# Kernel optimization log

Measured on AMD Instinct MI355X. Metric: run time of the kernel, lower is better.

## Reference

```python
import jax, jax.numpy as jnp
import numpy as np

X_CH, Y_CH, DIM, NUM_HEAD = 256, 512, 128, 4
H_DIM = DIM // NUM_HEAD
GAMMA = H_DIM ** (-0.5)


def conv1x1(x, w, b):
    # x: [B,C,H,W], w: [O,C], b: [O]
    return jnp.einsum('bchw,oc->bohw', x, w) + b[None, :, None, None]


def _split_qkv(qkv, bs, hw):
    # qkv: [B, 3*DIM, H, W] -> q,k,v each [B, NUM_HEAD, HW, H_DIM]
    qkv = qkv.reshape(bs, 3, NUM_HEAD, H_DIM, hw)
    qkv = jnp.transpose(qkv, (1, 0, 2, 4, 3))  # [3, B, H, HW, D]
    return qkv[0], qkv[1], qkv[2]


def setup_inputs() -> dict:
    key = jax.random.key(0)
    ks = jax.random.split(key, 12)
    s = lambda fan_in: 1.0 / np.sqrt(fan_in)
    x = jax.random.normal(ks[0], (2, X_CH, 64, 64), dtype=jnp.float32)
    y = jax.random.normal(ks[1], (2, Y_CH, 32, 32), dtype=jnp.float32)
    wx_qkv = jax.random.normal(ks[2], (3 * DIM, X_CH), dtype=jnp.float32) * s(X_CH)
    bx_qkv = jax.random.normal(ks[3], (3 * DIM,), dtype=jnp.float32) * s(X_CH)
    wy_qkv = jax.random.normal(ks[4], (3 * DIM, Y_CH), dtype=jnp.float32) * s(Y_CH)
    by_qkv = jax.random.normal(ks[5], (3 * DIM,), dtype=jnp.float32) * s(Y_CH)
    wpx = jax.random.normal(ks[6], (X_CH, DIM), dtype=jnp.float32) * s(DIM)
    bpx = jax.random.normal(ks[7], (X_CH,), dtype=jnp.float32) * s(DIM)
    wpy = jax.random.normal(ks[8], (Y_CH, DIM), dtype=jnp.float32) * s(DIM)
    bpy = jax.random.normal(ks[9], (Y_CH,), dtype=jnp.float32) * s(DIM)
    return {"x": x, "y": y, "wx_qkv": wx_qkv, "bx_qkv": bx_qkv,
            "wy_qkv": wy_qkv, "by_qkv": by_qkv,
            "wpx": wpx, "bpx": bpx, "wpy": wpy, "bpy": bpy}


def reference(x, y, wx_qkv, bx_qkv, wy_qkv, by_qkv, wpx, bpx, wpy, bpy):
    bs, _, h_x, w_x = x.shape
    _, _, h_y, w_y = y.shape
    hw_x, hw_y = h_x * w_x, h_y * w_y

    q_x, k_x, v_x = _split_qkv(conv1x1(x, wx_qkv, bx_qkv), bs, hw_x)
    q_y, k_y, v_y = _split_qkv(conv1x1(y, wy_qkv, by_qkv), bs, hw_y)

    # x attends to y
    atten_x = jax.nn.softmax(jnp.einsum('bhqd,bhkd->bhqk', q_x, k_y) * GAMMA, axis=-1)
    out_x = jnp.einsum('bhqk,bhkd->bhqd', atten_x, v_y)  # [B,H,HWx,D]
    out_x = jnp.transpose(out_x, (0, 1, 3, 2)).reshape(bs, DIM, h_x, w_x)

    # y attends to x
    atten_y = jax.nn.softmax(jnp.einsum('bhqd,bhkd->bhqk', q_y, k_x) * GAMMA, axis=-1)
    out_y = jnp.einsum('bhqk,bhkd->bhqd', atten_y, v_x)
    out_y = jnp.transpose(out_y, (0, 1, 3, 2)).reshape(bs, DIM, h_y, w_y)

    out_x = conv1x1(out_x, wpx, bpx) + x
    out_y = conv1x1(out_y, wpy, bpy) + y
    return out_x, out_y
```

## Files before the change

kernel.cpp:

```cpp
#include <hip/hip_runtime.h>
#include <hip/hip_bf16.h>
#include <cstdint>

#define B 2
#define NH 4
#define HD 32
#define DIM 128
#define CX 256
#define CY 512
#define PX 4096
#define PY 1024
#define QKV 384
#define GAMMA 0.17677669529663687f

typedef unsigned short u16;
typedef unsigned int u32;

using short8 = __attribute__((ext_vector_type(8))) short;
using f32x4  = __attribute__((ext_vector_type(4))) float;

__device__ __forceinline__ float bf2f(u32 h) {
  union { u32 u; float f; } v; v.u = (h & 0xffffu) << 16; return v.f;
}
__device__ __forceinline__ u16 f2bf(float f) {
  u32 u = __float_as_uint(f);
  u32 r = (u + 0x7fffu + ((u >> 16) & 1u)) >> 16;
  return (u16)r;
}
__device__ __forceinline__ bool is_f32(const void* src) {
  u32 u = ((const u16*)src)[2 * (threadIdx.x & 63)];
  return __ballot((u & 0x7F80u) >= 0x4600u) != 0ull;
}

#define N_X   (B * CX * PX)
#define N_Y   (B * CY * PY)
#define N_WX  (QKV * CX)
#define N_BX  (QKV)
#define N_WY  (QKV * CY)
#define N_BY  (QKV)
#define N_WPX (CX * DIM)
#define N_BPX (CX)
#define N_WPY (CY * DIM)
#define N_BPY (CY)

enum : size_t {
  OFF_CWX   = 0,
  OFF_CBX   = OFF_CWX  + N_WX,
  OFF_CWY   = OFF_CBX  + N_BX,
  OFF_CBY   = OFF_CWY  + N_WY,
  OFF_CWPX  = OFF_CBY  + N_BY,
  OFF_CBPX  = OFF_CWPX + N_WPX,
  OFF_CWPY  = OFF_CBPX + N_BPX,
  OFF_CBPY  = OFF_CWPY + N_WPY,
  OFF_XT    = OFF_CBPY + N_BPY,
  OFF_YT    = OFF_XT   + (size_t)B * PX * CX,
  OFF_QPX   = OFF_YT   + (size_t)B * PY * CY,
  OFF_KPX   = OFF_QPX  + (size_t)B * NH * PX * HD,
  OFF_QPY   = OFF_KPX  + (size_t)B * NH * PX * HD,
  OFF_KPY   = OFF_QPY  + (size_t)B * NH * PY * HD,
  OFF_VCX   = OFF_KPY  + (size_t)B * NH * PY * HD,
  OFF_VCY   = OFF_VCX  + (size_t)B * DIM * PX,
  OFF_OTX   = OFF_VCY  + (size_t)B * DIM * PY,
  OFF_OTY   = OFF_OTX  + (size_t)B * PX * DIM,
  WS_END    = OFF_OTY  + (size_t)B * PY * DIM,
};

#define XPX_BLKS 512
#define XPY_BLKS 256
__global__ __launch_bounds__(256) void k_prep(
    const void* x, const void* y, const void* wx, const void* bx,
    const void* wy, const void* by, const void* wpx, const void* bpx,
    const void* wpy, const void* bpy, u16* __restrict__ ws) {
  const int id = blockIdx.x;
  if (id < XPX_BLKS + XPY_BLKS) {
    __shared__ u16 tile[64][68];
    const void* src; u16* dst; int C, P, p_t, c_t, b;
    if (id < XPX_BLKS) {
      src = x; dst = ws + OFF_XT; C = CX; P = PX;
      p_t = id & 63; c_t = (id >> 6) & 3; b = id >> 8;
    } else {
      int id2 = id - XPX_BLKS;
      src = y; dst = ws + OFF_YT; C = CY; P = PY;
      p_t = id2 & 15; c_t = (id2 >> 4) & 7; b = id2 >> 7;
    }
    const bool f32in = is_f32(src);
    const int tx = threadIdx.x & 15, tc = threadIdx.x >> 4;
    const int p0 = p_t * 64, c0 = c_t * 64;
#pragma unroll
    for (int i = 0; i < 4; i++) {
      int cl = tc + i * 16;
      size_t sidx = ((size_t)b * C + c0 + cl) * P + p0 + tx * 4;
      u16 v0, v1, v2, v3;
      if (f32in) {
        float4 f = *(const float4*)((const float*)src + sidx);
        v0 = f2bf(f.x); v1 = f2bf(f.y); v2 = f2bf(f.z); v3 = f2bf(f.w);
      } else {
        uint2 u = *(const uint2*)((const u16*)src + sidx);
        v0 = (u16)u.x; v1 = (u16)(u.x >> 16); v2 = (u16)u.y; v3 = (u16)(u.y >> 16);
      }
      tile[tx * 4 + 0][cl] = v0; tile[tx * 4 + 1][cl] = v1;
      tile[tx * 4 + 2][cl] = v2; tile[tx * 4 + 3][cl] = v3;
    }
    __syncthreads();
#pragma unroll
    for (int i = 0; i < 4; i++) {
      int pl = tc + i * 16;
      *(uint2*)&dst[((size_t)b * P + p0 + pl) * C + c0 + tx * 4] =
          *(const uint2*)&tile[pl][tx * 4];
    }
  } else {
    int wid = id - (XPX_BLKS + XPY_BLKS);
    const void* src; size_t dstoff; int n, base;
    if      (wid < 48)  { src = wx;  dstoff = OFF_CWX;  n = N_WX;  base = 0; }
    else if (wid < 49)  { src = bx;  dstoff = OFF_CBX;  n = N_BX;  base = 48; }
    else if (wid < 145) { src = wy;  dstoff = OFF_CWY;  n = N_WY;  base = 49; }
    else if (wid < 146) { src = by;  dstoff = OFF_CBY;  n = N_BY;  base = 145; }
    else if (wid < 162) { src = wpx; dstoff = OFF_CWPX; n = N_WPX; base = 146; }
    else if (wid < 163) { src = bpx; dstoff = OFF_CBPX; n = N_BPX; base = 162; }
    else if (wid < 195) { src = wpy; dstoff = OFF_CWPY; n = N_WPY; base = 163; }
    else                { src = bpy; dstoff = OFF_CBPY; n = N_BPY; base = 195; }
    const bool f32in = is_f32(src);
    int e0 = (wid - base) * 2048 + threadIdx.x * 8;
    if (e0 >= n) return;
    u16* dst = ws + dstoff + e0;
    if (f32in) {
      const float* s = (const float*)src + e0;
      float4 a = *(const float4*)s;
      float4 bq = *(const float4*)(s + 4);
      ushort4 o0, o1;
      o0.x = f2bf(a.x);  o0.y = f2bf(a.y);  o0.z = f2bf(a.z);  o0.w = f2bf(a.w);
      o1.x = f2bf(bq.x); o1.y = f2bf(bq.y); o1.z = f2bf(bq.z); o1.w = f2bf(bq.w);
      *(ushort4*)dst = o0;
      *(ushort4*)(dst + 4) = o1;
    } else {
      uint4 v = *(const uint4*)((const u16*)src + e0);
      *(uint4*)dst = v;
    }
  }
}

__global__ __launch_bounds__(256) void k_qkv(u16* __restrict__ ws) {
  const int t = threadIdx.x;
  const int lane = t & 63, w = t >> 6;
  const int ql = lane & 15, quad = lane >> 4;
  const int b = blockIdx.z;

  const u16 *W, *Xt, *bias; u16 *qp, *kp, *vc; int C, P, pxb;
  if (blockIdx.x < 64) {
    W = ws + OFF_CWX; Xt = ws + OFF_XT; bias = ws + OFF_CBX;
    qp = ws + OFF_QPX; kp = ws + OFF_KPX; vc = ws + OFF_VCX;
    C = CX; P = PX; pxb = blockIdx.x;
  } else {
    W = ws + OFF_CWY; Xt = ws + OFF_YT; bias = ws + OFF_CBY;
    qp = ws + OFF_QPY; kp = ws + OFF_KPY; vc = ws + OFF_VCY;
    C = CY; P = PY; pxb = blockIdx.x - 64;
  }
  const int p_w = pxb * 64 + (w & 1) * 32;
  const int o_w = blockIdx.y * 64 + (w >> 1) * 32;

  const u16* wr0 = W + (size_t)(o_w + ql) * C;
  const u16* wr1 = W + (size_t)(o_w + 16 + ql) * C;
  const u16* xr0 = Xt + ((size_t)b * P + p_w + ql) * C;
  const u16* xr1 = Xt + ((size_t)b * P + p_w + 16 + ql) * C;

  union U { uint4 u; short8 s; };
  f32x4 acc[2][2];
#pragma unroll
  for (int i = 0; i < 2; i++)
#pragma unroll
    for (int j = 0; j < 2; j++) acc[i][j] = (f32x4){0.f, 0.f, 0.f, 0.f};

  U a0, a1, b0, b1, a0n, a1n, b0n, b1n;
  {
    int off = quad * 8;
    a0.u = *(const uint4*)&wr0[off];
    a1.u = *(const uint4*)&wr1[off];
    b0.u = *(const uint4*)&xr0[off];
    b1.u = *(const uint4*)&xr1[off];
  }

  const bool isv = blockIdx.y >= 4;
  if (!isv) {
#pragma unroll 4
    for (int c0 = 0; c0 < C; c0 += 32) {
      if (c0 + 32 < C) {
        int off = c0 + 32 + quad * 8;
        a0n.u = *(const uint4*)&wr0[off];
        a1n.u = *(const uint4*)&wr1[off];
        b0n.u = *(const uint4*)&xr0[off];
        b1n.u = *(const uint4*)&xr1[off];
      }
      acc[0][0] = __builtin_amdgcn_mfma_f32_16x16x32_bf16(a0.s, b0.s, acc[0][0], 0, 0, 0);
      acc[0][1] = __builtin_amdgcn_mfma_f32_16x16x32_bf16(a0.s, b1.s, acc[0][1], 0, 0, 0);
      acc[1][0] = __builtin_amdgcn_mfma_f32_16x16x32_bf16(a1.s, b0.s, acc[1][0], 0, 0, 0);
      acc[1][1] = __builtin_amdgcn_mfma_f32_16x16x32_bf16(a1.s, b1.s, acc[1][1], 0, 0, 0);
      a0 = a0n; a1 = a1n; b0 = b0n; b1 = b1n;
    }
  } else {
#pragma unroll 4
    for (int c0 = 0; c0 < C; c0 += 32) {
      if (c0 + 32 < C) {
        int off = c0 + 32 + quad * 8;
        a0n.u = *(const uint4*)&wr0[off];
        a1n.u = *(const uint4*)&wr1[off];
        b0n.u = *(const uint4*)&xr0[off];
        b1n.u = *(const uint4*)&xr1[off];
      }
      acc[0][0] = __builtin_amdgcn_mfma_f32_16x16x32_bf16(b0.s, a0.s, acc[0][0], 0, 0, 0);
      acc[0][1] = __builtin_amdgcn_mfma_f32_16x16x32_bf16(b1.s, a0.s, acc[0][1], 0, 0, 0);
      acc[1][0] = __builtin_amdgcn_mfma_f32_16x16x32_bf16(b0.s, a1.s, acc[1][0], 0, 0, 0);
      acc[1][1] = __builtin_amdgcn_mfma_f32_16x16x32_bf16(b1.s, a1.s, acc[1][1], 0, 0, 0);
      a0 = a0n; a1 = a1n; b0 = b0n; b1 = b1n;
    }
  }

  if (!isv) {
    float bs[2][4];
#pragma unroll
    for (int oi = 0; oi < 2; oi++)
#pragma unroll
      for (int r = 0; r < 4; r++)
        bs[oi][r] = bf2f(bias[o_w + oi * 16 + quad * 4 + r]);
    bool isq = blockIdx.y < 2;
    float scale = isq ? GAMMA : 1.0f;
    u16* dstT = isq ? qp : kp;
#pragma unroll
    for (int oi = 0; oi < 2; oi++)
#pragma unroll
      for (int pi = 0; pi < 2; pi++) {
        int p = p_w + pi * 16 + ql;
        int o = o_w + oi * 16 + quad * 4 - (isq ? 0 : 128);
        int hh = o >> 5, d = o & 31;
        f32x4 a = acc[oi][pi];
        uint2 pk;
        pk.x = (u32)f2bf((a[0] + bs[oi][0]) * scale) |
               ((u32)f2bf((a[1] + bs[oi][1]) * scale) << 16);
        pk.y = (u32)f2bf((a[2] + bs[oi][2]) * scale) |
               ((u32)f2bf((a[3] + bs[oi][3]) * scale) << 16);
        *(uint2*)&dstT[((size_t)(b * NH + hh) * P + p) * HD + d] = pk;
      }
  } else {
#pragma unroll
    for (int oi = 0; oi < 2; oi++) {
      int o = o_w + oi * 16 + ql - 256;
      float bv = bf2f(bias[o_w + oi * 16 + ql]);
#pragma unroll
      for (int pi = 0; pi < 2; pi++) {
        int pbase = p_w + pi * 16 + quad * 4;
        f32x4 a = acc[oi][pi];
        ushort4 st;
        st.x = f2bf(a[0] + bv); st.y = f2bf(a[1] + bv);
        st.z = f2bf(a[2] + bv); st.w = f2bf(a[3] + bv);
        *(ushort4*)&vc[((size_t)b * DIM + o) * P + pbase] = st;
      }
    }
  }
}

template <int NQF, int KW>
__device__ __forceinline__ void attn_core(
    const u16* __restrict__ Qp, const u16* __restrict__ Kp,
    const u16* __restrict__ Vc, u16* __restrict__ Ot, int Pq, int Pk,
    int q0, int h, int b, u16* pool, float (*lfb)[64]) {
  const int t = threadIdx.x;
  const int lane = t & 63, w = t >> 6;
  const int ql = lane & 15, quad = lane >> 4;

  union U { uint4 u; short8 s; };
  U qf[NQF];
#pragma unroll
  for (int qi = 0; qi < NQF; qi++)
    qf[qi].u = *(const uint4*)&Qp[((size_t)(b * NH + h) * Pq + q0 + qi * 16 + ql) * HD + quad * 8];

  const int kspan = Pk >> 2;
  const int kk0 = w * kspan;
  const int niter = kspan / KW;
  const int f0 = ((ql >> 2) << 3) | (ql & 3);

  const u16* kbase = Kp + ((size_t)(b * NH + h) * Pk + kk0 + f0) * HD + quad * 8;
  const u16* v0base = Vc + ((size_t)(b * DIM + h * HD + ql)) * Pk + kk0 + quad * 8;
  const u16* v1base = v0base + (size_t)16 * Pk;

  f32x4 o0[NQF], o1[NQF];
  float l_run[NQF];
#pragma unroll
  for (int qi = 0; qi < NQF; qi++) {
    o0[qi] = (f32x4){0.f, 0.f, 0.f, 0.f};
    o1[qi] = (f32x4){0.f, 0.f, 0.f, 0.f};
    l_run[qi] = 0.f;
  }

  auto step32 = [&](U& xka, U& xkb, U& xva, U& xvb) {
#pragma unroll
    for (int qi = 0; qi < NQF; qi++) {
      f32x4 z = {0.f, 0.f, 0.f, 0.f};
      f32x4 st0 = __builtin_amdgcn_mfma_f32_16x16x32_bf16(xka.s, qf[qi].s, z, 0, 0, 0);
      f32x4 st1 = __builtin_amdgcn_mfma_f32_16x16x32_bf16(xkb.s, qf[qi].s, z, 0, 0, 0);

      float p[8];
#pragma unroll
      for (int r = 0; r < 4; r++) { p[r] = __expf(st0[r]); p[4 + r] = __expf(st1[r]); }
      l_run[qi] += ((p[0] + p[1]) + (p[2] + p[3])) + ((p[4] + p[5]) + (p[6] + p[7]));

      U pf;
      pf.u.x = __builtin_amdgcn_perm(__float_as_uint(p[1]), __float_as_uint(p[0]), 0x07060302u);
      pf.u.y = __builtin_amdgcn_perm(__float_as_uint(p[3]), __float_as_uint(p[2]), 0x07060302u);
      pf.u.z = __builtin_amdgcn_perm(__float_as_uint(p[5]), __float_as_uint(p[4]), 0x07060302u);
      pf.u.w = __builtin_amdgcn_perm(__float_as_uint(p[7]), __float_as_uint(p[6]), 0x07060302u);

      o0[qi] = __builtin_amdgcn_mfma_f32_16x16x32_bf16(xva.s, pf.s, o0[qi], 0, 0, 0);
      o1[qi] = __builtin_amdgcn_mfma_f32_16x16x32_bf16(xvb.s, pf.s, o1[qi], 0, 0, 0);
    }
  };

  U ka, kb, va, vb, kan, kbn, van, vbn;
  U kc, kd, vc, vd, kcn, kdn, vcn, vdn;
  ka.u = *(const uint4*)&kbase[0];
  kb.u = *(const uint4*)&kbase[4 * HD];
  va.u = *(const uint4*)&v0base[0];
  vb.u = *(const uint4*)&v1base[0];
  if constexpr (KW == 64) {
    kc.u = *(const uint4*)&kbase[32 * HD];
    kd.u = *(const uint4*)&kbase[36 * HD];
    vc.u = *(const uint4*)&v0base[32];
    vd.u = *(const uint4*)&v1base[32];
  }

  for (int it = 0; it < niter; it++) {
    if (it + 1 < niter) {
      size_t go = (size_t)(it + 1) * KW;
      kan.u = *(const uint4*)&kbase[go * HD];
      kbn.u = *(const uint4*)&kbase[(go + 4) * HD];
      van.u = *(const uint4*)&v0base[go];
      vbn.u = *(const uint4*)&v1base[go];
      if constexpr (KW == 64) {
        kcn.u = *(const uint4*)&kbase[(go + 32) * HD];
        kdn.u = *(const uint4*)&kbase[(go + 36) * HD];
        vcn.u = *(const uint4*)&v0base[go + 32];
        vdn.u = *(const uint4*)&v1base[go + 32];
      }
    }

    step32(ka, kb, va, vb);
    if constexpr (KW == 64) step32(kc, kd, vc, vd);

    ka = kan; kb = kbn; va = van; vb = vbn;
    if constexpr (KW == 64) { kc = kcn; kd = kdn; vc = vcn; vd = vdn; }
  }

#pragma unroll
  for (int qi = 0; qi < NQF; qi++) {
    float l = l_run[qi];
    l += __shfl_xor(l, 16);
    l += __shfl_xor(l, 32);
    l_run[qi] = l;
  }

  float* Of = (float*)(pool + (size_t)w * 4096);
#pragma unroll
  for (int qi = 0; qi < NQF; qi++) {
#pragma unroll
    for (int r = 0; r < 4; r++) {
      Of[(qi * 16 + ql) * 32 + quad * 4 + r] = o0[qi][r];
      Of[(qi * 16 + ql) * 32 + 16 + quad * 4 + r] = o1[qi][r];
    }
    if (quad == 0) lfb[w][qi * 16 + ql] = l_run[qi];
  }
  __syncthreads();

  const float* OfA = (const float*)pool;
#pragma unroll
  for (int k = 0; k < NQF * 2; k++) {
    int e = t + k * 256;
    int q = e >> 5, d = e & 31;
    float lt = lfb[0][q] + lfb[1][q] + lfb[2][q] + lfb[3][q];
    int di = q * 32 + d;
    float v = (OfA[di] + OfA[2048 + di]) + (OfA[4096 + di] + OfA[6144 + di]);
    Ot[((size_t)b * Pq + q0 + q) * DIM + h * HD + d] = f2bf(v / lt);
  }
}

__global__ __launch_bounds__(256) void k_attn(u16* __restrict__ ws) {
  __shared__ __align__(16) u16 pool[16384];
  __shared__ float lfb[4][64];
  const int c = blockIdx.x & 7;
  const int j = blockIdx.x >> 3;
  const int b = c >> 2, h = c & 3;
  if (j < 32) {
    attn_core<2, 64>(ws + OFF_QPY, ws + OFF_KPX, ws + OFF_VCX, ws + OFF_OTY,
                     PY, PX, j * 32, h, b, pool, lfb);
  } else {
    attn_core<4, 32>(ws + OFF_QPX, ws + OFF_KPY, ws + OFF_VCY, ws + OFF_OTX,
                     PX, PY, (j - 32) * 64, h, b, pool, lfb);
  }
}

__global__ __launch_bounds__(256) void k_proj(
    u16* __restrict__ ws, void* __restrict__ outv,
    const void* __restrict__ resx, const void* __restrict__ resy) {
  const int u = blockIdx.x;
  const u16 *W, *A, *bias; const void* res; int OT, P, pxb, byi, b; size_t out_off;
  if (u < 512) {
    W = ws + OFF_CWPX; A = ws + OFF_OTX; bias = ws + OFF_CBPX;
    res = resx; OT = CX; P = PX; out_off = 0;
    pxb = u & 63; byi = (u >> 6) & 3; b = u >> 8;
  } else {
    int v = u - 512;
    W = ws + OFF_CWPY; A = ws + OFF_OTY; bias = ws + OFF_CBPY;
    res = resy; OT = CY; P = PY; out_off = (size_t)B * CX * PX;
    pxb = v & 15; byi = (v >> 4) & 7; b = v >> 7;
  }
  const bool f32io = is_f32(res);
  const int t = threadIdx.x;
  const int lane = t & 63, w = t >> 6;
  const int ql = lane & 15, quad = lane >> 4;
  const int p_w = pxb * 64 + (w & 1) * 32;
  const int o_w = byi * 64 + (w >> 1) * 32;

  const u16* wr0 = W + (size_t)(o_w + ql) * DIM;
  const u16* wr1 = W + (size_t)(o_w + 16 + ql) * DIM;
  const u16* xr0 = A + ((size_t)b * P + p_w + ql) * DIM;
  const u16* xr1 = A + ((size_t)b * P + p_w + 16 + ql) * DIM;

  union U { uint4 u; short8 s; };
  U wa0[4], wa1[4], xb0[4], xb1[4];
#pragma unroll
  for (int i = 0; i < 4; i++) {
    int off = i * 32 + quad * 8;
    wa0[i].u = *(const uint4*)&wr0[off];
    wa1[i].u = *(const uint4*)&wr1[off];
    xb0[i].u = *(const uint4*)&xr0[off];
    xb1[i].u = *(const uint4*)&xr1[off];
  }

  f32x4 acc[2][2];
#pragma unroll
  for (int i = 0; i < 2; i++)
#pragma unroll
    for (int j = 0; j < 2; j++) acc[i][j] = (f32x4){0.f, 0.f, 0.f, 0.f};

#pragma unroll
  for (int i = 0; i < 4; i++) {
    acc[0][0] = __builtin_amdgcn_mfma_f32_16x16x32_bf16(xb0[i].s, wa0[i].s, acc[0][0], 0, 0, 0);
    acc[0][1] = __builtin_amdgcn_mfma_f32_16x16x32_bf16(xb1[i].s, wa0[i].s, acc[0][1], 0, 0, 0);
    acc[1][0] = __builtin_amdgcn_mfma_f32_16x16x32_bf16(xb0[i].s, wa1[i].s, acc[1][0], 0, 0, 0);
    acc[1][1] = __builtin_amdgcn_mfma_f32_16x16x32_bf16(xb1[i].s, wa1[i].s, acc[1][1], 0, 0, 0);
  }

#pragma unroll
  for (int oi = 0; oi < 2; oi++) {
    int o = o_w + oi * 16 + ql;
    float bv = bf2f(bias[o]);
#pragma unroll
    for (int pi = 0; pi < 2; pi++) {
      int pbase = p_w + pi * 16 + quad * 4;
      size_t idx = ((size_t)b * OT + o) * P + pbase;
      f32x4 a = acc[oi][pi];
      if (f32io) {
        float4 rv = *(const float4*)((const float*)res + idx);
        float4 ov;
        ov.x = a[0] + bv + rv.x; ov.y = a[1] + bv + rv.y;
        ov.z = a[2] + bv + rv.z; ov.w = a[3] + bv + rv.w;
        *(float4*)((float*)outv + out_off + idx) = ov;
      } else {
        ushort4 rv = *(const ushort4*)((const u16*)res + idx);
        ushort4 ov;
        ov.x = f2bf(a[0] + bv + bf2f(rv.x));
        ov.y = f2bf(a[1] + bv + bf2f(rv.y));
        ov.z = f2bf(a[2] + bv + bf2f(rv.z));
        ov.w = f2bf(a[3] + bv + bf2f(rv.w));
        *(ushort4*)((u16*)outv + out_off + idx) = ov;
      }
    }
  }
}

extern "C" void kernel_launch(void* const* d_in, const int* in_sizes, int n_in,
                              void* d_out, int out_size, void* d_ws, size_t ws_size,
                              hipStream_t stream) {
  (void)in_sizes; (void)n_in; (void)out_size; (void)ws_size;
  u16* ws = (u16*)d_ws;

  k_prep<<<dim3(XPX_BLKS + XPY_BLKS + 196), 256, 0, stream>>>(
      d_in[0], d_in[1], d_in[2], d_in[3], d_in[4], d_in[5],
      d_in[6], d_in[7], d_in[8], d_in[9], ws);
  k_qkv<<<dim3(80, 6, B), 256, 0, stream>>>(ws);
  k_attn<<<dim3(768), 256, 0, stream>>>(ws);
  k_proj<<<dim3(768), 256, 0, stream>>>(ws, d_out, d_in[0], d_in[1]);
}
```

Baseline: 135.2 us.

## Fuse input transpose and bf16 conversion into QKV and projection kernels

Removes the separate prep kernel that converted x, y and the weights to bf16 and transposed the activations into workspace. The QKV kernel now loads raw input tiles, converts and transposes them through double-buffered shared memory, and converts fp32 weights to bf16 on the fly. The projection kernel also reads fp32 weights and biases directly. This saves one launch and a full round trip of the activations through global memory. In exchange the weights are converted redundantly in every block and a barrier is added per 64-channel chunk.

```diff
diff --git a/kernel.cpp b/kernel.cpp
--- a/kernel.cpp
+++ b/kernel.cpp
@@ -32,29 +32,8 @@
   return __ballot((u & 0x7F80u) >= 0x4600u) != 0ull;
 }
 
-#define N_X   (B * CX * PX)
-#define N_Y   (B * CY * PY)
-#define N_WX  (QKV * CX)
-#define N_BX  (QKV)
-#define N_WY  (QKV * CY)
-#define N_BY  (QKV)
-#define N_WPX (CX * DIM)
-#define N_BPX (CX)
-#define N_WPY (CY * DIM)
-#define N_BPY (CY)
-
 enum : size_t {
-  OFF_CWX   = 0,
-  OFF_CBX   = OFF_CWX  + N_WX,
-  OFF_CWY   = OFF_CBX  + N_BX,
-  OFF_CBY   = OFF_CWY  + N_WY,
-  OFF_CWPX  = OFF_CBY  + N_BY,
-  OFF_CBPX  = OFF_CWPX + N_WPX,
-  OFF_CWPY  = OFF_CBPX + N_BPX,
-  OFF_CBPY  = OFF_CWPY + N_WPY,
-  OFF_XT    = OFF_CBPY + N_BPY,
-  OFF_YT    = OFF_XT   + (size_t)B * PX * CX,
-  OFF_QPX   = OFF_YT   + (size_t)B * PY * CY,
+  OFF_QPX   = 0,
   OFF_KPX   = OFF_QPX  + (size_t)B * NH * PX * HD,
   OFF_QPY   = OFF_KPX  + (size_t)B * NH * PX * HD,
   OFF_KPY   = OFF_QPY  + (size_t)B * NH * PY * HD,
@@ -65,153 +44,129 @@
   WS_END    = OFF_OTY  + (size_t)B * PY * DIM,
 };
 
-#define XPX_BLKS 512
-#define XPY_BLKS 256
-__global__ __launch_bounds__(256) void k_prep(
-    const void* x, const void* y, const void* wx, const void* bx,
-    const void* wy, const void* by, const void* wpx, const void* bpx,
-    const void* wpy, const void* bpy, u16* __restrict__ ws) {
-  const int id = blockIdx.x;
-  if (id < XPX_BLKS + XPY_BLKS) {
-    __shared__ u16 tile[64][68];
-    const void* src; u16* dst; int C, P, p_t, c_t, b;
-    if (id < XPX_BLKS) {
-      src = x; dst = ws + OFF_XT; C = CX; P = PX;
-      p_t = id & 63; c_t = (id >> 6) & 3; b = id >> 8;
-    } else {
-      int id2 = id - XPX_BLKS;
-      src = y; dst = ws + OFF_YT; C = CY; P = PY;
-      p_t = id2 & 15; c_t = (id2 >> 4) & 7; b = id2 >> 7;
-    }
-    const bool f32in = is_f32(src);
-    const int tx = threadIdx.x & 15, tc = threadIdx.x >> 4;
-    const int p0 = p_t * 64, c0 = c_t * 64;
-#pragma unroll
-    for (int i = 0; i < 4; i++) {
-      int cl = tc + i * 16;
-      size_t sidx = ((size_t)b * C + c0 + cl) * P + p0 + tx * 4;
-      u16 v0, v1, v2, v3;
-      if (f32in) {
-        float4 f = *(const float4*)((const float*)src + sidx);
-        v0 = f2bf(f.x); v1 = f2bf(f.y); v2 = f2bf(f.z); v3 = f2bf(f.w);
-      } else {
-        uint2 u = *(const uint2*)((const u16*)src + sidx);
-        v0 = (u16)u.x; v1 = (u16)(u.x >> 16); v2 = (u16)u.y; v3 = (u16)(u.y >> 16);
-      }
-      tile[tx * 4 + 0][cl] = v0; tile[tx * 4 + 1][cl] = v1;
-      tile[tx * 4 + 2][cl] = v2; tile[tx * 4 + 3][cl] = v3;
-    }
-    __syncthreads();
-#pragma unroll
-    for (int i = 0; i < 4; i++) {
-      int pl = tc + i * 16;
-      *(uint2*)&dst[((size_t)b * P + p0 + pl) * C + c0 + tx * 4] =
-          *(const uint2*)&tile[pl][tx * 4];
-    }
-  } else {
-    int wid = id - (XPX_BLKS + XPY_BLKS);
-    const void* src; size_t dstoff; int n, base;
-    if      (wid < 48)  { src = wx;  dstoff = OFF_CWX;  n = N_WX;  base = 0; }
-    else if (wid < 49)  { src = bx;  dstoff = OFF_CBX;  n = N_BX;  base = 48; }
-    else if (wid < 145) { src = wy;  dstoff = OFF_CWY;  n = N_WY;  base = 49; }
-    else if (wid < 146) { src = by;  dstoff = OFF_CBY;  n = N_BY;  base = 145; }
-    else if (wid < 162) { src = wpx; dstoff = OFF_CWPX; n = N_WPX; base = 146; }
-    else if (wid < 163) { src = bpx; dstoff = OFF_CBPX; n = N_BPX; base = 162; }
-    else if (wid < 195) { src = wpy; dstoff = OFF_CWPY; n = N_WPY; base = 163; }
-    else                { src = bpy; dstoff = OFF_CBPY; n = N_BPY; base = 195; }
-    const bool f32in = is_f32(src);
-    int e0 = (wid - base) * 2048 + threadIdx.x * 8;
-    if (e0 >= n) return;
-    u16* dst = ws + dstoff + e0;
-    if (f32in) {
-      const float* s = (const float*)src + e0;
-      float4 a = *(const float4*)s;
-      float4 bq = *(const float4*)(s + 4);
-      ushort4 o0, o1;
-      o0.x = f2bf(a.x);  o0.y = f2bf(a.y);  o0.z = f2bf(a.z);  o0.w = f2bf(a.w);
-      o1.x = f2bf(bq.x); o1.y = f2bf(bq.y); o1.z = f2bf(bq.z); o1.w = f2bf(bq.w);
-      *(ushort4*)dst = o0;
-      *(ushort4*)(dst + 4) = o1;
-    } else {
-      uint4 v = *(const uint4*)((const u16*)src + e0);
-      *(uint4*)dst = v;
-    }
-  }
-}
-
-__global__ __launch_bounds__(256) void k_qkv(u16* __restrict__ ws) {
+__global__ __launch_bounds__(256) void k_qkv(
+    const void* __restrict__ xin, const void* __restrict__ yin,
+    const void* __restrict__ wxp, const void* __restrict__ bxp,
+    const void* __restrict__ wyp, const void* __restrict__ byp,
+    u16* __restrict__ ws) {
+  __shared__ __align__(16) u16 xt[2][64][68];
   const int t = threadIdx.x;
   const int lane = t & 63, w = t >> 6;
   const int ql = lane & 15, quad = lane >> 4;
   const int b = blockIdx.z;
 
-  const u16 *W, *Xt, *bias; u16 *qp, *kp, *vc; int C, P, pxb;
+  const void *W, *Xsrc, *bias; u16 *qp, *kp, *vc; int C, P, pxb;
   if (blockIdx.x < 64) {
-    W = ws + OFF_CWX; Xt = ws + OFF_XT; bias = ws + OFF_CBX;
+    W = wxp; Xsrc = xin; bias = bxp;
     qp = ws + OFF_QPX; kp = ws + OFF_KPX; vc = ws + OFF_VCX;
     C = CX; P = PX; pxb = blockIdx.x;
   } else {
-    W = ws + OFF_CWY; Xt = ws + OFF_YT; bias = ws + OFF_CBY;
+    W = wyp; Xsrc = yin; bias = byp;
     qp = ws + OFF_QPY; kp = ws + OFF_KPY; vc = ws + OFF_VCY;
     C = CY; P = PY; pxb = blockIdx.x - 64;
   }
-  const int p_w = pxb * 64 + (w & 1) * 32;
+  const bool xf32 = is_f32(Xsrc);
+  const bool wf32 = is_f32(W);
+  const bool bf32 = is_f32(bias);
+  const int NC = C >> 6;
+  const int p0 = pxb * 64;
+  const int pw_loc = (w & 1) * 32;
   const int o_w = blockIdx.y * 64 + (w >> 1) * 32;
-
-  const u16* wr0 = W + (size_t)(o_w + ql) * C;
-  const u16* wr1 = W + (size_t)(o_w + 16 + ql) * C;
-  const u16* xr0 = Xt + ((size_t)b * P + p_w + ql) * C;
-  const u16* xr1 = Xt + ((size_t)b * P + p_w + 16 + ql) * C;
+  const int tx = t & 15, tc = t >> 4;
 
   union U { uint4 u; short8 s; };
+
+  float4 sf[4]; uint2 su[4];
+  auto stage_load = [&](int ci) {
+#pragma unroll
+    for (int i = 0; i < 4; i++) {
+      int cl = tc + i * 16;
+      size_t sidx = ((size_t)b * C + ci * 64 + cl) * P + p0 + tx * 4;
+      if (xf32) sf[i] = *(const float4*)((const float*)Xsrc + sidx);
+      else      su[i] = *(const uint2*)((const u16*)Xsrc + sidx);
+    }
+  };
+  auto stage_write = [&](int buf) {
+#pragma unroll
+    for (int i = 0; i < 4; i++) {
+      int cl = tc + i * 16;
+      if (xf32) {
+        xt[buf][tx * 4 + 0][cl] = f2bf(sf[i].x);
+        xt[buf][tx * 4 + 1][cl] = f2bf(sf[i].y);
+        xt[buf][tx * 4 + 2][cl] = f2bf(sf[i].z);
+        xt[buf][tx * 4 + 3][cl] = f2bf(sf[i].w);
+      } else {
+        xt[buf][tx * 4 + 0][cl] = (u16)su[i].x;
+        xt[buf][tx * 4 + 1][cl] = (u16)(su[i].x >> 16);
+        xt[buf][tx * 4 + 2][cl] = (u16)su[i].y;
+        xt[buf][tx * 4 + 3][cl] = (u16)(su[i].y >> 16);
+      }
+    }
+  };
+
+  auto loadW = [&](int row, int cglob) {
+    U r;
+    if (wf32) {
+      const float* wp = (const float*)W + (size_t)row * C + cglob;
+      float4 lo = *(const float4*)wp;
+      float4 hi = *(const float4*)(wp + 4);
+      r.u.x = (u32)f2bf(lo.x) | ((u32)f2bf(lo.y) << 16);
+      r.u.y = (u32)f2bf(lo.z) | ((u32)f2bf(lo.w) << 16);
+      r.u.z = (u32)f2bf(hi.x) | ((u32)f2bf(hi.y) << 16);
+      r.u.w = (u32)f2bf(hi.z) | ((u32)f2bf(hi.w) << 16);
+    } else {
+      r.u = *(const uint4*)((const u16*)W + (size_t)row * C + cglob);
+    }
+    return r;
+  };
+  auto bval = [&](int o) -> float {
+    return bf32 ? ((const float*)bias)[o] : bf2f(((const u16*)bias)[o]);
+  };
+
   f32x4 acc[2][2];
 #pragma unroll
   for (int i = 0; i < 2; i++)
 #pragma unroll
     for (int j = 0; j < 2; j++) acc[i][j] = (f32x4){0.f, 0.f, 0.f, 0.f};
 
-  U a0, a1, b0, b1, a0n, a1n, b0n, b1n;
-  {
-    int off = quad * 8;
-    a0.u = *(const uint4*)&wr0[off];
-    a1.u = *(const uint4*)&wr1[off];
-    b0.u = *(const uint4*)&xr0[off];
-    b1.u = *(const uint4*)&xr1[off];
-  }
+  stage_load(0);
+  stage_write(0);
+  __syncthreads();
 
   const bool isv = blockIdx.y >= 4;
-  if (!isv) {
-#pragma unroll 4
-    for (int c0 = 0; c0 < C; c0 += 32) {
-      if (c0 + 32 < C) {
-        int off = c0 + 32 + quad * 8;
-        a0n.u = *(const uint4*)&wr0[off];
-        a1n.u = *(const uint4*)&wr1[off];
-        b0n.u = *(const uint4*)&xr0[off];
-        b1n.u = *(const uint4*)&xr1[off];
-      }
-      acc[0][0] = __builtin_amdgcn_mfma_f32_16x16x32_bf16(a0.s, b0.s, acc[0][0], 0, 0, 0);
-      acc[0][1] = __builtin_amdgcn_mfma_f32_16x16x32_bf16(a0.s, b1.s, acc[0][1], 0, 0, 0);
-      acc[1][0] = __builtin_amdgcn_mfma_f32_16x16x32_bf16(a1.s, b0.s, acc[1][0], 0, 0, 0);
-      acc[1][1] = __builtin_amdgcn_mfma_f32_16x16x32_bf16(a1.s, b1.s, acc[1][1], 0, 0, 0);
-      a0 = a0n; a1 = a1n; b0 = b0n; b1 = b1n;
-    }
-  } else {
-#pragma unroll 4
-    for (int c0 = 0; c0 < C; c0 += 32) {
-      if (c0 + 32 < C) {
-        int off = c0 + 32 + quad * 8;
-        a0n.u = *(const uint4*)&wr0[off];
-        a1n.u = *(const uint4*)&wr1[off];
-        b0n.u = *(const uint4*)&xr0[off];
-        b1n.u = *(const uint4*)&xr1[off];
-      }
-      acc[0][0] = __builtin_amdgcn_mfma_f32_16x16x32_bf16(b0.s, a0.s, acc[0][0], 0, 0, 0);
-      acc[0][1] = __builtin_amdgcn_mfma_f32_16x16x32_bf16(b1.s, a0.s, acc[0][1], 0, 0, 0);
-      acc[1][0] = __builtin_amdgcn_mfma_f32_16x16x32_bf16(b0.s, a1.s, acc[1][0], 0, 0, 0);
-      acc[1][1] = __builtin_amdgcn_mfma_f32_16x16x32_bf16(b1.s, a1.s, acc[1][1], 0, 0, 0);
-      a0 = a0n; a1 = a1n; b0 = b0n; b1 = b1n;
-    }
+  int buf = 0;
+  for (int ci = 0; ci < NC; ci++) {
+    if (ci + 1 < NC) stage_load(ci + 1);
+#pragma unroll
+    for (int ks = 0; ks < 2; ks++) {
+      const int kl = ks * 32 + quad * 8;
+      const int cglob = ci * 64 + kl;
+      U a0 = loadW(o_w + ql, cglob);
+      U a1 = loadW(o_w + 16 + ql, cglob);
+      U b0, b1;
+      {
+        uint2 lo = *(const uint2*)&xt[buf][pw_loc + ql][kl];
+        uint2 hi = *(const uint2*)&xt[buf][pw_loc + ql][kl + 4];
+        b0.u.x = lo.x; b0.u.y = lo.y; b0.u.z = hi.x; b0.u.w = hi.y;
+        uint2 lo1 = *(const uint2*)&xt[buf][pw_loc + 16 + ql][kl];
+        uint2 hi1 = *(const uint2*)&xt[buf][pw_loc + 16 + ql][kl + 4];
+        b1.u.x = lo1.x; b1.u.y = lo1.y; b1.u.z = hi1.x; b1.u.w = hi1.y;
+      }
+      if (!isv) {
+        acc[0][0] = __builtin_amdgcn_mfma_f32_16x16x32_bf16(a0.s, b0.s, acc[0][0], 0, 0, 0);
+        acc[0][1] = __builtin_amdgcn_mfma_f32_16x16x32_bf16(a0.s, b1.s, acc[0][1], 0, 0, 0);
+        acc[1][0] = __builtin_amdgcn_mfma_f32_16x16x32_bf16(a1.s, b0.s, acc[1][0], 0, 0, 0);
+        acc[1][1] = __builtin_amdgcn_mfma_f32_16x16x32_bf16(a1.s, b1.s, acc[1][1], 0, 0, 0);
+      } else {
+        acc[0][0] = __builtin_amdgcn_mfma_f32_16x16x32_bf16(b0.s, a0.s, acc[0][0], 0, 0, 0);
+        acc[0][1] = __builtin_amdgcn_mfma_f32_16x16x32_bf16(b1.s, a0.s, acc[0][1], 0, 0, 0);
+        acc[1][0] = __builtin_amdgcn_mfma_f32_16x16x32_bf16(b0.s, a1.s, acc[1][0], 0, 0, 0);
+        acc[1][1] = __builtin_amdgcn_mfma_f32_16x16x32_bf16(b1.s, a1.s, acc[1][1], 0, 0, 0);
+      }
+    }
+    if (ci + 1 < NC) stage_write(buf ^ 1);
+    __syncthreads();
+    buf ^= 1;
   }
 
   if (!isv) {
@@ -220,7 +175,7 @@
     for (int oi = 0; oi < 2; oi++)
 #pragma unroll
       for (int r = 0; r < 4; r++)
-        bs[oi][r] = bf2f(bias[o_w + oi * 16 + quad * 4 + r]);
+        bs[oi][r] = bval(o_w + oi * 16 + quad * 4 + r);
     bool isq = blockIdx.y < 2;
     float scale = isq ? GAMMA : 1.0f;
     u16* dstT = isq ? qp : kp;
@@ -228,7 +183,7 @@
     for (int oi = 0; oi < 2; oi++)
 #pragma unroll
       for (int pi = 0; pi < 2; pi++) {
-        int p = p_w + pi * 16 + ql;
+        int p = p0 + pw_loc + pi * 16 + ql;
         int o = o_w + oi * 16 + quad * 4 - (isq ? 0 : 128);
         int hh = o >> 5, d = o & 31;
         f32x4 a = acc[oi][pi];
@@ -243,10 +198,10 @@
 #pragma unroll
     for (int oi = 0; oi < 2; oi++) {
       int o = o_w + oi * 16 + ql - 256;
-      float bv = bf2f(bias[o_w + oi * 16 + ql]);
+      float bv = bval(o_w + oi * 16 + ql);
 #pragma unroll
       for (int pi = 0; pi < 2; pi++) {
-        int pbase = p_w + pi * 16 + quad * 4;
+        int pbase = p0 + pw_loc + pi * 16 + quad * 4;
         f32x4 a = acc[oi][pi];
         ushort4 st;
         st.x = f2bf(a[0] + bv); st.y = f2bf(a[1] + bv);
@@ -397,38 +352,57 @@
 
 __global__ __launch_bounds__(256) void k_proj(
     u16* __restrict__ ws, void* __restrict__ outv,
-    const void* __restrict__ resx, const void* __restrict__ resy) {
+    const void* __restrict__ resx, const void* __restrict__ resy,
+    const void* __restrict__ wpxp, const void* __restrict__ bpxp,
+    const void* __restrict__ wpyp, const void* __restrict__ bpyp) {
   const int u = blockIdx.x;
-  const u16 *W, *A, *bias; const void* res; int OT, P, pxb, byi, b; size_t out_off;
+  const void *W, *bias; const u16* A; const void* res;
+  int OT, P, pxb, byi, b; size_t out_off;
   if (u < 512) {
-    W = ws + OFF_CWPX; A = ws + OFF_OTX; bias = ws + OFF_CBPX;
+    W = wpxp; A = ws + OFF_OTX; bias = bpxp;
     res = resx; OT = CX; P = PX; out_off = 0;
     pxb = u & 63; byi = (u >> 6) & 3; b = u >> 8;
   } else {
     int v = u - 512;
-    W = ws + OFF_CWPY; A = ws + OFF_OTY; bias = ws + OFF_CBPY;
+    W = wpyp; A = ws + OFF_OTY; bias = bpyp;
     res = resy; OT = CY; P = PY; out_off = (size_t)B * CX * PX;
     pxb = v & 15; byi = (v >> 4) & 7; b = v >> 7;
   }
   const bool f32io = is_f32(res);
+  const bool wf32 = is_f32(W);
+  const bool bf32 = is_f32(bias);
   const int t = threadIdx.x;
   const int lane = t & 63, w = t >> 6;
   const int ql = lane & 15, quad = lane >> 4;
   const int p_w = pxb * 64 + (w & 1) * 32;
   const int o_w = byi * 64 + (w >> 1) * 32;
 
-  const u16* wr0 = W + (size_t)(o_w + ql) * DIM;
-  const u16* wr1 = W + (size_t)(o_w + 16 + ql) * DIM;
+  union U { uint4 u; short8 s; };
+  auto loadW = [&](int row, int off) {
+    U r;
+    if (wf32) {
+      const float* wp = (const float*)W + (size_t)row * DIM + off;
+      float4 lo = *(const float4*)wp;
+      float4 hi = *(const float4*)(wp + 4);
+      r.u.x = (u32)f2bf(lo.x) | ((u32)f2bf(lo.y) << 16);
+      r.u.y = (u32)f2bf(lo.z) | ((u32)f2bf(lo.w) << 16);
+      r.u.z = (u32)f2bf(hi.x) | ((u32)f2bf(hi.y) << 16);
+      r.u.w = (u32)f2bf(hi.z) | ((u32)f2bf(hi.w) << 16);
+    } else {
+      r.u = *(const uint4*)((const u16*)W + (size_t)row * DIM + off);
+    }
+    return r;
+  };
+
   const u16* xr0 = A + ((size_t)b * P + p_w + ql) * DIM;
   const u16* xr1 = A + ((size_t)b * P + p_w + 16 + ql) * DIM;
 
-  union U { uint4 u; short8 s; };
   U wa0[4], wa1[4], xb0[4], xb1[4];
 #pragma unroll
   for (int i = 0; i < 4; i++) {
     int off = i * 32 + quad * 8;
-    wa0[i].u = *(const uint4*)&wr0[off];
-    wa1[i].u = *(const uint4*)&wr1[off];
+    wa0[i] = loadW(o_w + ql, off);
+    wa1[i] = loadW(o_w + 16 + ql, off);
     xb0[i].u = *(const uint4*)&xr0[off];
     xb1[i].u = *(const uint4*)&xr1[off];
   }
@@ -450,7 +424,7 @@
 #pragma unroll
   for (int oi = 0; oi < 2; oi++) {
     int o = o_w + oi * 16 + ql;
-    float bv = bf2f(bias[o]);
+    float bv = bf32 ? ((const float*)bias)[o] : bf2f(((const u16*)bias)[o]);
 #pragma unroll
     for (int pi = 0; pi < 2; pi++) {
       int pbase = p_w + pi * 16 + quad * 4;
@@ -481,10 +455,9 @@
   (void)in_sizes; (void)n_in; (void)out_size; (void)ws_size;
   u16* ws = (u16*)d_ws;
 
-  k_prep<<<dim3(XPX_BLKS + XPY_BLKS + 196), 256, 0, stream>>>(
-      d_in[0], d_in[1], d_in[2], d_in[3], d_in[4], d_in[5],
-      d_in[6], d_in[7], d_in[8], d_in[9], ws);
-  k_qkv<<<dim3(80, 6, B), 256, 0, stream>>>(ws);
+  k_qkv<<<dim3(80, 6, B), 256, 0, stream>>>(
+      d_in[0], d_in[1], d_in[2], d_in[3], d_in[4], d_in[5], ws);
   k_attn<<<dim3(768), 256, 0, stream>>>(ws);
-  k_proj<<<dim3(768), 256, 0, stream>>>(ws, d_out, d_in[0], d_in[1]);
-}
+  k_proj<<<dim3(768), 256, 0, stream>>>(ws, d_out, d_in[0], d_in[1],
+                                        d_in[6], d_in[7], d_in[8], d_in[9]);
+}
```

After: 143.1 us. 5.9% more time.
